# Optimization experiments

Measured on AMD Instinct MI355X. Metric: run time of the kernel, lower is better.

## Reference

```python
import jax, jax.numpy as jnp
import numpy as np

NUM_PER_SCALE = (64, 64, 64)   # static num_intervals_per_scale
DIST_BINS = 21
NUM_CLASSES = 5
D = 128   # node_embedding_dim
N = 512   # number of nodes (time frames)
KSIZE = 5


def _gru_last(x_seq, lens, Wih, Whh, bih, bhh):
    """Masked GRU over padded seqs; final hidden at each sequence's true length.
    x_seq: [I, T, F], lens: [I]. PyTorch GRU cell math."""
    I, T, _ = x_seq.shape
    H = Whh.shape[1]
    mask_t = (jnp.arange(T)[None, :] < lens[:, None]).T  # [T, I]

    def step(h, inp):
        x_t, m = inp
        gi = x_t @ Wih.T + bih            # [I, 3H]
        gh = h @ Whh.T + bhh
        ir, iz, in_ = jnp.split(gi, 3, axis=-1)
        hr, hz, hn = jnp.split(gh, 3, axis=-1)
        r = jax.nn.sigmoid(ir + hr)
        z = jax.nn.sigmoid(iz + hz)
        n = jnp.tanh(in_ + r * hn)
        h_new = (1.0 - z) * n + z * h
        return jnp.where(m[:, None], h_new, h), None

    h0 = jnp.zeros((I, H), x_seq.dtype)
    h_fin, _ = jax.lax.scan(step, h0, (jnp.swapaxes(x_seq, 0, 1), mask_t))
    return h_fin


def _bigru_last(x_pad, lens, Wih, Whh, bih, bhh):
    """Bidirectional GRU final hiddens, matching packed-sequence semantics."""
    hf = _gru_last(x_pad, lens, Wih[0], Whh[0], bih[0], bhh[0])
    T = x_pad.shape[1]
    t = jnp.arange(T)[None, :]
    rev = jnp.where(t < lens[:, None], lens[:, None] - 1 - t, t)  # reverse within valid length
    x_rev = jnp.take_along_axis(x_pad, rev[:, :, None], axis=1)
    hb = _gru_last(x_rev, lens, Wih[1], Whh[1], bih[1], bhh[1])
    return hf, hb


def reference(node_embeddings, time_positions, node_pred, audio_len,
              cur_anchor_intervals, smooth_kernel,
              feat_Wih, feat_Whh, feat_bih, feat_bhh,
              abn_Wih, abn_Whh, abn_bih, abn_bhh,
              start_w, end_w,
              uni_W1, uni_b1, uni_W2, uni_b2, uni_W3, uni_b3):
    n, d = node_embeddings.shape
    al = audio_len
    # temporal encoding
    freqs = jnp.linspace(0.0, 10.0, d)
    x = node_embeddings + 0.05 * jnp.sin(time_positions * freqs)  # [N, D]
    # grouped gaussian smoothing over time per class channel (symmetric kernel)
    pad = KSIZE // 2
    xp = jnp.pad(node_pred, ((pad, pad), (0, 0)))
    win = jnp.stack([xp[k:k + n] for k in range(KSIZE)])          # [K, N, C]
    smoothed = jax.nn.softmax(jnp.einsum('k,knc->nc', smooth_kernel, win), axis=-1)
    abnormal = smoothed[:, 0]                                     # normal_class_idx = 0
    tpos = time_positions[:, 0] * al                              # [N]

    bounds_list, conf_list, cls_list = [], [], []
    off = 0
    for s in range(3):
        ni = NUM_PER_SCALE[s]
        anc = cur_anchor_intervals[off:off + ni]
        off += ni
        starts, ends = anc[:, 0], anc[:, 1]
        mask = (tpos[None, :] >= starts[:, None]) & (tpos[None, :] <= ends[:, None])  # [ni, N]
        lens = mask.sum(axis=1)
        # stable gather: in-interval nodes first, original node order preserved
        key = jnp.where(mask, 0, n) + jnp.arange(n)[None, :]
        order = jnp.argsort(key, axis=1)
        x_pad = x[order]                       # [ni, N, D]
        abn_pad = abnormal[order][:, :, None]  # [ni, N, 1]
        hf, hb = _bigru_last(x_pad, lens, feat_Wih[s], feat_Whh[s], feat_bih[s], feat_bhh[s])
        af, ab = _bigru_last(abn_pad, lens, abn_Wih[s], abn_Whh[s], abn_bih[s], abn_bhh[s])
        local_feat = jnp.concatenate([hf, hb], axis=1)             # [ni, 2D]
        local_abn = (af[:, 0] + ab[:, 0]) * 0.5
        centers = (starts + ends) * 0.5
        widths = ends - starts
        sf = jnp.concatenate([local_feat, local_abn[:, None],
                              (centers / al)[:, None], (widths / al)[:, None]], axis=1)
        h = jax.nn.relu(sf @ uni_W1[s] + uni_b1[s])
        h = jax.nn.relu(h @ uni_W2[s] + uni_b2[s])   # dropout inactive (eval)
        out = h @ uni_W3[s] + uni_b3[s]
        sl = out[:, :DIST_BINS]
        el = out[:, DIST_BINS:2 * DIST_BINS]
        conf = out[:, 2 * DIST_BINS]
        cls = out[:, 2 * DIST_BINS + 1:]
        so = jax.nn.softmax(sl, axis=1) @ start_w[s]
        eo = jax.nn.softmax(el, axis=1) @ end_w[s]
        st = jnp.clip(starts + so, 0.0, al)
        en = jnp.clip(ends + eo, 0.0, al)
        bounds_list.append(jnp.stack([st, en], axis=1))
        conf_list.append(conf)
        cls_list.append(cls)
    return (jnp.concatenate(bounds_list, 0),
            jnp.concatenate(conf_list, 0),
            jnp.concatenate(cls_list, 0))


def setup_inputs():
    key = jax.random.key(0)
    ks = jax.random.split(key, 16)
    node_embeddings = jax.random.normal(ks[0], (N, D), dtype=jnp.float32)
    time_positions = jax.random.uniform(ks[1], (N, 1), dtype=jnp.float32)
    node_pred = jax.random.normal(ks[2], (N, NUM_CLASSES), dtype=jnp.float32)
    audio_len = jnp.ones((), jnp.float32)
    total = sum(NUM_PER_SCALE)
    st = jax.random.uniform(ks[3], (total,), minval=0.0, maxval=0.75)
    wd = jax.random.uniform(ks[4], (total,), minval=0.05, maxval=0.2)
    cur_anchor_intervals = jnp.stack([st, jnp.minimum(st + wd, 1.0)], axis=1)
    smooth_kernel = jnp.array([0.06136, 0.24477, 0.38774, 0.24477, 0.06136], jnp.float32)
    feat_Wih = 0.05 * jax.random.normal(ks[5], (3, 2, 3 * D, D))
    feat_Whh = 0.05 * jax.random.normal(ks[6], (3, 2, 3 * D, D))
    feat_bih = 0.05 * jax.random.normal(ks[7], (3, 2, 3 * D))
    feat_bhh = 0.05 * jax.random.normal(ks[8], (3, 2, 3 * D))
    abn_Wih = 0.5 * jax.random.normal(ks[9], (3, 2, 3, 1))
    abn_Whh = 0.5 * jax.random.normal(ks[10], (3, 2, 3, 1))
    abn_bih = 0.5 * jax.random.normal(ks[11], (3, 2, 3))
    abn_bhh = 0.5 * jax.random.normal(ks[12], (3, 2, 3))
    lin = jnp.linspace(-20.0, 20.0, DIST_BINS)
    start_w = jnp.tile(lin[None, :], (3, 1))
    end_w = jnp.tile(lin[None, :], (3, 1))
    fin = 2 * D + 3
    fout = 2 * DIST_BINS + 1 + (NUM_CLASSES - 1)
    uni_W1 = jax.random.normal(ks[13], (3, fin, 256)) / float(np.sqrt(fin))
    uni_b1 = jnp.zeros((3, 256), jnp.float32)
    uni_W2 = jax.random.normal(ks[14], (3, 256, 256)) / 16.0
    uni_b2 = jnp.zeros((3, 256), jnp.float32)
    uni_W3 = jax.random.normal(ks[15], (3, 256, fout)) / 16.0
    uni_b3 = jnp.zeros((3, fout), jnp.float32)
    return dict(node_embeddings=node_embeddings, time_positions=time_positions,
                node_pred=node_pred, audio_len=audio_len,
                cur_anchor_intervals=cur_anchor_intervals, smooth_kernel=smooth_kernel,
                feat_Wih=feat_Wih, feat_Whh=feat_Whh, feat_bih=feat_bih, feat_bhh=feat_bhh,
                abn_Wih=abn_Wih, abn_Whh=abn_Whh, abn_bih=abn_bih, abn_bhh=abn_bhh,
                start_w=start_w, end_w=end_w,
                uni_W1=uni_W1, uni_b1=uni_b1, uni_W2=uni_W2, uni_b2=uni_b2,
                uni_W3=uni_W3, uni_b3=uni_b3)
```

## Files before the change

### kernel.cpp

```cpp
#include <hip/hip_runtime.h>
#include <math.h>

#define N_NODES 512
#define DIM 128
#define NANCH 192
#define G3 384
#define FOUT 47
#define DBINS 21

__device__ __forceinline__ float fast_sigmoid(float x) {
    return __builtin_amdgcn_rcpf(1.f + __expf(-x));
}
__device__ __forceinline__ float fast_tanh(float x) {
    return 1.f - 2.f * __builtin_amdgcn_rcpf(1.f + __expf(2.f * x));
}

__global__ __launch_bounds__(384) void prep_kernel(
    const float* __restrict__ emb, const float* __restrict__ tpin,
    const float* __restrict__ Wih, const float* __restrict__ bih,
    const float* __restrict__ alp, const float* __restrict__ anchors,
    const float* __restrict__ npred, const float* __restrict__ skern,
    const float* __restrict__ aWih, const float* __restrict__ aWhh,
    const float* __restrict__ abih, const float* __restrict__ abhh,
    float* __restrict__ xW, int* __restrict__ members,
    int* __restrict__ lens, float* __restrict__ abn_res)
{
    int blk = blockIdx.x;
    int tid = threadIdx.x;
    if (blk < 192) {
        int sd = blk >> 5;
        int ng = blk & 31;
        __shared__ __align__(16) float xs[16][DIM];
        for (int idx = tid; idx < 16 * DIM; idx += 384) {
            int m = idx >> 7, k = idx & 127;
            int node = ng * 16 + m;
            float tv = tpin[node];
            float freq = 10.f * (float)k / 127.f;
            xs[m][k] = emb[node * DIM + k] + 0.05f * __sinf(tv * freq);
        }
        __syncthreads();
        float acc[16];
        float b = bih[sd * G3 + tid];
        #pragma unroll
        for (int m = 0; m < 16; ++m) acc[m] = b;
        const float* wrow = Wih + ((size_t)sd * G3 + tid) * DIM;
        for (int k = 0; k < DIM; k += 4) {
            float4 w4 = *(const float4*)(wrow + k);
            #pragma unroll
            for (int m = 0; m < 16; ++m) {
                float4 xv = *(const float4*)&xs[m][k];
                acc[m] = fmaf(w4.x, xv.x, acc[m]);
                acc[m] = fmaf(w4.y, xv.y, acc[m]);
                acc[m] = fmaf(w4.z, xv.z, acc[m]);
                acc[m] = fmaf(w4.w, xv.w, acc[m]);
            }
        }
        #pragma unroll
        for (int m = 0; m < 16; ++m)
            xW[((size_t)sd * N_NODES + ng * 16 + m) * G3 + tid] = acc[m];
    } else {
        int a = blk - 192;
        float al = alp[0];
        float s0 = anchors[a * 2 + 0];
        float e0 = anchors[a * 2 + 1];
        __shared__ int memloc[N_NODES];
        __shared__ float abn_lds[N_NODES];
        for (int node = tid; node < N_NODES; node += 384) {
            float sc[5];
            #pragma unroll
            for (int ch = 0; ch < 5; ++ch) {
                float acc = 0.f;
                #pragma unroll
                for (int k = 0; k < 5; ++k) {
                    int r = node + k - 2;
                    if (r >= 0 && r < N_NODES) acc += skern[k] * npred[r * 5 + ch];
                }
                sc[ch] = acc;
            }
            float m = sc[0];
            #pragma unroll
            for (int ch = 1; ch < 5; ++ch) m = fmaxf(m, sc[ch]);
            float sum = 0.f;
            #pragma unroll
            for (int ch = 0; ch < 5; ++ch) sum += __expf(sc[ch] - m);
            abn_lds[node] = __expf(sc[0] - m) / sum;
        }
        __syncthreads();
        if (tid < 64) {
            int lane = tid;
            int count = 0;
            for (int c = 0; c < N_NODES / 64; ++c) {
                int node = c * 64 + lane;
                float tp = tpin[node] * al;
                bool in = (tp >= s0) && (tp <= e0);
                unsigned long long m = __ballot(in);
                if (in) {
                    int pos = count + __popcll(m & ((1ull << lane) - 1ull));
                    members[a * N_NODES + pos] = node;
                    memloc[pos] = node;
                }
                count += __popcll(m);
            }
            if (lane == 0) lens[a] = count;
            int sc3 = a >> 6;
            float h = 0.f;
            if (lane < 2) {
                int sd = sc3 * 2 + lane;
                float wi0 = aWih[sd*3+0], wi1 = aWih[sd*3+1], wi2 = aWih[sd*3+2];
                float wh0 = aWhh[sd*3+0], wh1 = aWhh[sd*3+1], wh2 = aWhh[sd*3+2];
                float bi0 = abih[sd*3+0], bi1 = abih[sd*3+1], bi2 = abih[sd*3+2];
                float bh0 = abhh[sd*3+0], bh1 = abhh[sd*3+1], bh2 = abhh[sd*3+2];
                for (int t = 0; t < count; ++t) {
                    int idx = lane ? (count - 1 - t) : t;
                    float xv = abn_lds[memloc[idx]];
                    float r = fast_sigmoid(fmaf(wi0, xv, bi0) + fmaf(wh0, h, bh0));
                    float z = fast_sigmoid(fmaf(wi1, xv, bi1) + fmaf(wh1, h, bh1));
                    float nv = fast_tanh(fmaf(wi2, xv, bi2) + r * fmaf(wh2, h, bh2));
                    h = (1.f - z) * nv + z * h;
                }
            }
            float hb = __shfl(h, 1);
            if (lane == 0) abn_res[a] = 0.5f * (h + hb);
        }
    }
}

__global__ __launch_bounds__(512, 1) void gru_feat_kernel(
    const float* __restrict__ xW, const float* __restrict__ Whh,
    const float* __restrict__ bhh, const int* __restrict__ members,
    const int* __restrict__ lens, const float* __restrict__ anchors,
    float* __restrict__ feat_out)
{
    int b = blockIdx.x;
    int t0 = threadIdx.x;
    int j  = t0 >> 2;
    int s  = t0 & 3;

    __shared__ int perm_l[NANCH];
    if (t0 < NANCH) {
        float w = anchors[2 * t0 + 1] - anchors[2 * t0];
        int rank = 0;
        for (int q = 0; q < NANCH; ++q) {
            float wq = anchors[2 * q + 1] - anchors[2 * q];
            rank += (wq > w) || (wq == w && q < t0);
        }
        perm_l[rank] = t0;
    }
    __syncthreads();
    int a   = perm_l[b >> 1];
    int dir = b & 1;
    int sd  = (a >> 6) * 2 + dir;

    float wr[32], wz[32], wn[32];
    {
        const float* base = Whh + ((size_t)sd * G3) * DIM;
        const float* pr = base + (size_t)(j        ) * DIM + s * 32;
        const float* pz = base + (size_t)(j + DIM  ) * DIM + s * 32;
        const float* pn = base + (size_t)(j + 2*DIM) * DIM + s * 32;
        #pragma unroll
        for (int q = 0; q < 8; ++q) {
            float4 v = *(const float4*)(pr + 4 * q);
            wr[4*q+0]=v.x; wr[4*q+1]=v.y; wr[4*q+2]=v.z; wr[4*q+3]=v.w;
        }
        #pragma unroll
        for (int q = 0; q < 8; ++q) {
            float4 v = *(const float4*)(pz + 4 * q);
            wz[4*q+0]=v.x; wz[4*q+1]=v.y; wz[4*q+2]=v.z; wz[4*q+3]=v.w;
        }
        #pragma unroll
        for (int q = 0; q < 8; ++q) {
            float4 v = *(const float4*)(pn + 4 * q);
            wn[4*q+0]=v.x; wn[4*q+1]=v.y; wn[4*q+2]=v.z; wn[4*q+3]=v.w;
        }
    }
    #pragma unroll
    for (int q = 0; q < 32; ++q)
        asm volatile("" : "+v"(wr[q]), "+v"(wz[q]), "+v"(wn[q]));

    float bhr = bhh[sd * G3 + j];
    float bhz = bhh[sd * G3 + DIM + j];
    float bhn = bhh[sd * G3 + 2 * DIM + j];

    const float* xWp = xW + (size_t)sd * N_NODES * G3;
    const int* mem = members + a * N_NODES;
    int len = lens[a];

    __shared__ __align__(16) float hbuf[2][4][36];
    for (int i = t0; i < 2 * 4 * 36; i += 512) ((float*)hbuf)[i] = 0.f;
    __syncthreads();

    int node0 = (len > 0) ? mem[dir ? (len - 1) : 0] : 0;
    float gr = xWp[(size_t)node0 * G3 + j];
    float gz = xWp[(size_t)node0 * G3 + DIM + j];
    float gn = xWp[(size_t)node0 * G3 + 2 * DIM + j];

    int cur = 0;
    for (int t = 0; t < len; ++t) {
        float gr_n = 0.f, gz_n = 0.f, gn_n = 0.f;
        if (t + 1 < len) {
            int nn = mem[dir ? (len - 2 - t) : (t + 1)];
            gr_n = xWp[(size_t)nn * G3 + j];
            gz_n = xWp[(size_t)nn * G3 + DIM + j];
            gn_n = xWp[(size_t)nn * G3 + 2 * DIM + j];
        }
        float ar = 0.f, az = 0.f, an_ = 0.f;
        const float4* hp = (const float4*)(&hbuf[cur][s][0]);
        #pragma unroll
        for (int q = 0; q < 8; ++q) {
            float4 hv = hp[q];
            ar = fmaf(wr[4*q+0], hv.x, ar); ar = fmaf(wr[4*q+1], hv.y, ar);
            ar = fmaf(wr[4*q+2], hv.z, ar); ar = fmaf(wr[4*q+3], hv.w, ar);
            az = fmaf(wz[4*q+0], hv.x, az); az = fmaf(wz[4*q+1], hv.y, az);
            az = fmaf(wz[4*q+2], hv.z, az); az = fmaf(wz[4*q+3], hv.w, az);
            an_ = fmaf(wn[4*q+0], hv.x, an_); an_ = fmaf(wn[4*q+1], hv.y, an_);
            an_ = fmaf(wn[4*q+2], hv.z, an_); an_ = fmaf(wn[4*q+3], hv.w, an_);
        }
        ar  += __shfl_xor(ar, 1);  ar  += __shfl_xor(ar, 2);
        az  += __shfl_xor(az, 1);  az  += __shfl_xor(az, 2);
        an_ += __shfl_xor(an_, 1); an_ += __shfl_xor(an_, 2);

        float r  = fast_sigmoid(gr + ar + bhr);
        float z  = fast_sigmoid(gz + az + bhz);
        float nv = fast_tanh(gn + r * (an_ + bhn));
        float hj = hbuf[cur][j >> 5][j & 31];
        float hnew = (1.f - z) * nv + z * hj;
        if (s == 0) hbuf[cur ^ 1][j >> 5][j & 31] = hnew;
        __syncthreads();
        cur ^= 1;
        gr = gr_n; gz = gz_n; gn = gn_n;
    }
    if (s == 0) feat_out[a * 256 + dir * DIM + j] = hbuf[cur][j >> 5][j & 31];
}

__global__ __launch_bounds__(256) void head_kernel(
    const float* __restrict__ feat, const float* __restrict__ abn_res,
    const float* __restrict__ anchors, const float* __restrict__ alp,
    const float* __restrict__ W1, const float* __restrict__ b1,
    const float* __restrict__ W2, const float* __restrict__ b2,
    const float* __restrict__ W3, const float* __restrict__ b3,
    const float* __restrict__ sw, const float* __restrict__ ew,
    float* __restrict__ out)
{
    int a = blockIdx.x;
    int tid = threadIdx.x;
    int s = a >> 6;
    __shared__ float sf[260];
    __shared__ float h1[256];
    __shared__ float h2[256];
    __shared__ float o[FOUT];
    float al = alp[0];
    float st = anchors[a * 2 + 0];
    float en = anchors[a * 2 + 1];
    sf[tid] = feat[a * 256 + tid];
    if (tid == 0) {
        sf[256] = abn_res[a];
        sf[257] = (st + en) * 0.5f / al;
        sf[258] = (en - st) / al;
    }
    __syncthreads();

    const float* w1 = W1 + (size_t)s * 259 * 256;
    float acc = b1[s * 256 + tid];
    for (int jj = 0; jj < 259; ++jj) acc = fmaf(sf[jj], w1[jj * 256 + tid], acc);
    h1[tid] = fmaxf(acc, 0.f);
    __syncthreads();

    const float* w2 = W2 + (size_t)s * 256 * 256;
    acc = b2[s * 256 + tid];
    for (int jj = 0; jj < 256; ++jj) acc = fmaf(h1[jj], w2[jj * 256 + tid], acc);
    h2[tid] = fmaxf(acc, 0.f);
    __syncthreads();

    if (tid < FOUT) {
        const float* w3 = W3 + (size_t)s * 256 * FOUT;
        acc = b3[s * FOUT + tid];
        for (int jj = 0; jj < 256; ++jj) acc = fmaf(h2[jj], w3[jj * FOUT + tid], acc);
        o[tid] = acc;
    }
    __syncthreads();

    if (tid < 2) {
        const float* lw = (tid == 0) ? (sw + s * DBINS) : (ew + s * DBINS);
        const float* sl = o + tid * DBINS;
        float m = sl[0];
        for (int jj = 1; jj < DBINS; ++jj) m = fmaxf(m, sl[jj]);
        float sum = 0.f, dot = 0.f;
        for (int jj = 0; jj < DBINS; ++jj) {
            float e = __expf(sl[jj] - m);
            sum += e;
            dot = fmaf(e, lw[jj], dot);
        }
        float off = dot / sum;
        float base = (tid == 0) ? st : en;
        out[a * 2 + tid] = fminf(fmaxf(base + off, 0.f), al);
    }
    if (tid == 42) out[2 * NANCH + a] = o[42];
    if (tid >= 43 && tid < FOUT) out[3 * NANCH + a * 4 + (tid - 43)] = o[tid];
}

extern "C" void kernel_launch(void* const* d_in, const int* in_sizes, int n_in,
                              void* d_out, int out_size, void* d_ws, size_t ws_size,
                              hipStream_t stream) {
    const float* emb   = (const float*)d_in[0];
    const float* tpin  = (const float*)d_in[1];
    const float* npred = (const float*)d_in[2];
    const float* alp   = (const float*)d_in[3];
    const float* anch  = (const float*)d_in[4];
    const float* skern = (const float*)d_in[5];
    const float* fWih  = (const float*)d_in[6];
    const float* fWhh  = (const float*)d_in[7];
    const float* fbih  = (const float*)d_in[8];
    const float* fbhh  = (const float*)d_in[9];
    const float* aWih  = (const float*)d_in[10];
    const float* aWhh  = (const float*)d_in[11];
    const float* abih  = (const float*)d_in[12];
    const float* abhh  = (const float*)d_in[13];
    const float* sw    = (const float*)d_in[14];
    const float* ew    = (const float*)d_in[15];
    const float* W1    = (const float*)d_in[16];
    const float* b1    = (const float*)d_in[17];
    const float* W2    = (const float*)d_in[18];
    const float* b2    = (const float*)d_in[19];
    const float* W3    = (const float*)d_in[20];
    const float* b3    = (const float*)d_in[21];

    float* ws = (float*)d_ws;
    float* xW       = ws;
    float* abn_res  = ws + 1179648;
    float* feat     = ws + 1179904;
    int*   members  = (int*)(ws + 1229056);
    int*   lens     = (int*)(ws + 1327360);
    float* outp     = (float*)d_out;

    prep_kernel<<<384, 384, 0, stream>>>(emb, tpin, fWih, fbih, alp, anch, npred, skern,
                                         aWih, aWhh, abih, abhh,
                                         xW, members, lens, abn_res);
    gru_feat_kernel<<<2 * NANCH, 512, 0, stream>>>(xW, fWhh, fbhh, members, lens, anch, feat);
    head_kernel<<<NANCH, 256, 0, stream>>>(feat, abn_res, anch, alp,
                                           W1, b1, W2, b2, W3, b3, sw, ew, outp);
}
```

Before: 243.2 us.

## Batch two anchors per GRU block, staging recurrent weights in LDS

Each GRU block now processes two anchors of the same scale and direction, paired by width rank within their scale, so the per-step weight reads are shared across two hidden states. The r and z recurrent weights move from registers into padded LDS, and the n weights are re-read from global memory every step. The grid is halved to 192 blocks, and per-sequence length masking is added so paired sequences of different lengths run in lockstep. The aim is to halve the number of serial blocks and reuse weights, at the cost of more LDS and global traffic per step and wasted steps when the paired lengths differ.

```diff
diff --git a/kernel.cpp b/kernel.cpp
--- a/kernel.cpp
+++ b/kernel.cpp
@@ -7,6 +7,7 @@
 #define G3 384
 #define FOUT 47
 #define DBINS 21
+#define WPAD 132
 
 __device__ __forceinline__ float fast_sigmoid(float x) {
     return __builtin_amdgcn_rcpf(1.f + __expf(-x));
@@ -125,111 +126,141 @@
     }
 }
 
-__global__ __launch_bounds__(512, 1) void gru_feat_kernel(
+__global__ __launch_bounds__(512) void gru_feat_kernel(
     const float* __restrict__ xW, const float* __restrict__ Whh,
     const float* __restrict__ bhh, const int* __restrict__ members,
     const int* __restrict__ lens, const float* __restrict__ anchors,
     float* __restrict__ feat_out)
 {
-    int b = blockIdx.x;
+    int bb = blockIdx.x;
     int t0 = threadIdx.x;
     int j  = t0 >> 2;
     int s  = t0 & 3;
-
-    __shared__ int perm_l[NANCH];
-    if (t0 < NANCH) {
-        float w = anchors[2 * t0 + 1] - anchors[2 * t0];
+    int sc  = bb >> 6;
+    int idx = bb & 63;
+    int dir = idx & 1;
+    int pr  = idx >> 1;
+    int sd  = sc * 2 + dir;
+
+    __shared__ __align__(16) float ldsW[2 * DIM * WPAD];
+    __shared__ __align__(16) float hbA[2][4][36];
+    __shared__ __align__(16) float hbB[2][4][36];
+    __shared__ int perm_l[64];
+
+    if (t0 < 64) {
+        int aa = sc * 64 + t0;
+        float w = anchors[2 * aa + 1] - anchors[2 * aa];
         int rank = 0;
-        for (int q = 0; q < NANCH; ++q) {
-            float wq = anchors[2 * q + 1] - anchors[2 * q];
+        for (int q = 0; q < 64; ++q) {
+            int aq = sc * 64 + q;
+            float wq = anchors[2 * aq + 1] - anchors[2 * aq];
             rank += (wq > w) || (wq == w && q < t0);
         }
-        perm_l[rank] = t0;
-    }
-    __syncthreads();
-    int a   = perm_l[b >> 1];
-    int dir = b & 1;
-    int sd  = (a >> 6) * 2 + dir;
-
-    float wr[32], wz[32], wn[32];
-    {
-        const float* base = Whh + ((size_t)sd * G3) * DIM;
-        const float* pr = base + (size_t)(j        ) * DIM + s * 32;
-        const float* pz = base + (size_t)(j + DIM  ) * DIM + s * 32;
-        const float* pn = base + (size_t)(j + 2*DIM) * DIM + s * 32;
-        #pragma unroll
-        for (int q = 0; q < 8; ++q) {
-            float4 v = *(const float4*)(pr + 4 * q);
-            wr[4*q+0]=v.x; wr[4*q+1]=v.y; wr[4*q+2]=v.z; wr[4*q+3]=v.w;
-        }
-        #pragma unroll
-        for (int q = 0; q < 8; ++q) {
-            float4 v = *(const float4*)(pz + 4 * q);
-            wz[4*q+0]=v.x; wz[4*q+1]=v.y; wz[4*q+2]=v.z; wz[4*q+3]=v.w;
-        }
-        #pragma unroll
-        for (int q = 0; q < 8; ++q) {
-            float4 v = *(const float4*)(pn + 4 * q);
-            wn[4*q+0]=v.x; wn[4*q+1]=v.y; wn[4*q+2]=v.z; wn[4*q+3]=v.w;
-        }
-    }
-    #pragma unroll
-    for (int q = 0; q < 32; ++q)
-        asm volatile("" : "+v"(wr[q]), "+v"(wz[q]), "+v"(wn[q]));
+        perm_l[rank] = aa;
+    }
+    const float* wbase = Whh + (size_t)sd * G3 * DIM;
+    for (int i = t0; i < 2 * DIM * 32; i += 512) {
+        int row = i >> 5, c = (i & 31) << 2;
+        *(float4*)&ldsW[row * WPAD + c] = *(const float4*)(wbase + row * DIM + c);
+    }
+    for (int i = t0; i < 2 * 4 * 36; i += 512) { ((float*)hbA)[i] = 0.f; ((float*)hbB)[i] = 0.f; }
+    __syncthreads();
+
+    int a0 = perm_l[2 * pr], a1 = perm_l[2 * pr + 1];
 
     float bhr = bhh[sd * G3 + j];
     float bhz = bhh[sd * G3 + DIM + j];
     float bhn = bhh[sd * G3 + 2 * DIM + j];
 
     const float* xWp = xW + (size_t)sd * N_NODES * G3;
-    const int* mem = members + a * N_NODES;
-    int len = lens[a];
-
-    __shared__ __align__(16) float hbuf[2][4][36];
-    for (int i = t0; i < 2 * 4 * 36; i += 512) ((float*)hbuf)[i] = 0.f;
-    __syncthreads();
-
-    int node0 = (len > 0) ? mem[dir ? (len - 1) : 0] : 0;
-    float gr = xWp[(size_t)node0 * G3 + j];
-    float gz = xWp[(size_t)node0 * G3 + DIM + j];
-    float gn = xWp[(size_t)node0 * G3 + 2 * DIM + j];
+    const int* memA = members + a0 * N_NODES;  int lenA = lens[a0];
+    const int* memB = members + a1 * N_NODES;  int lenB = lens[a1];
+    int T = lenA > lenB ? lenA : lenB;
+
+    int n0A = (lenA > 0) ? memA[dir ? (lenA - 1) : 0] : 0;
+    float grA = xWp[(size_t)n0A * G3 + j];
+    float gzA = xWp[(size_t)n0A * G3 + DIM + j];
+    float gnA = xWp[(size_t)n0A * G3 + 2 * DIM + j];
+    int n0B = (lenB > 0) ? memB[dir ? (lenB - 1) : 0] : 0;
+    float grB = xWp[(size_t)n0B * G3 + j];
+    float gzB = xWp[(size_t)n0B * G3 + DIM + j];
+    float gnB = xWp[(size_t)n0B * G3 + 2 * DIM + j];
+
+    const float4* wr4 = (const float4*)&ldsW[(size_t)j * WPAD + s * 32];
+    const float4* wz4 = (const float4*)&ldsW[(size_t)(DIM + j) * WPAD + s * 32];
+    const float4* wnp = (const float4*)(wbase + (size_t)(2 * DIM + j) * DIM + s * 32);
 
     int cur = 0;
-    for (int t = 0; t < len; ++t) {
-        float gr_n = 0.f, gz_n = 0.f, gn_n = 0.f;
-        if (t + 1 < len) {
-            int nn = mem[dir ? (len - 2 - t) : (t + 1)];
-            gr_n = xWp[(size_t)nn * G3 + j];
-            gz_n = xWp[(size_t)nn * G3 + DIM + j];
-            gn_n = xWp[(size_t)nn * G3 + 2 * DIM + j];
-        }
-        float ar = 0.f, az = 0.f, an_ = 0.f;
-        const float4* hp = (const float4*)(&hbuf[cur][s][0]);
+    for (int t = 0; t < T; ++t) {
+        float4 wnv[8];
+        #pragma unroll
+        for (int q = 0; q < 8; ++q) wnv[q] = wnp[q];
+        float grA_n = 0.f, gzA_n = 0.f, gnA_n = 0.f;
+        float grB_n = 0.f, gzB_n = 0.f, gnB_n = 0.f;
+        if (t + 1 < lenA) {
+            int nn = memA[dir ? (lenA - 2 - t) : (t + 1)];
+            grA_n = xWp[(size_t)nn * G3 + j];
+            gzA_n = xWp[(size_t)nn * G3 + DIM + j];
+            gnA_n = xWp[(size_t)nn * G3 + 2 * DIM + j];
+        }
+        if (t + 1 < lenB) {
+            int nn = memB[dir ? (lenB - 2 - t) : (t + 1)];
+            grB_n = xWp[(size_t)nn * G3 + j];
+            gzB_n = xWp[(size_t)nn * G3 + DIM + j];
+            gnB_n = xWp[(size_t)nn * G3 + 2 * DIM + j];
+        }
+        float arA = 0.f, azA = 0.f, anA = 0.f, arB = 0.f, azB = 0.f, anB = 0.f;
+        const float4* hA4 = (const float4*)&hbA[cur][s][0];
+        const float4* hB4 = (const float4*)&hbB[cur][s][0];
         #pragma unroll
         for (int q = 0; q < 8; ++q) {
-            float4 hv = hp[q];
-            ar = fmaf(wr[4*q+0], hv.x, ar); ar = fmaf(wr[4*q+1], hv.y, ar);
-            ar = fmaf(wr[4*q+2], hv.z, ar); ar = fmaf(wr[4*q+3], hv.w, ar);
-            az = fmaf(wz[4*q+0], hv.x, az); az = fmaf(wz[4*q+1], hv.y, az);
-            az = fmaf(wz[4*q+2], hv.z, az); az = fmaf(wz[4*q+3], hv.w, az);
-            an_ = fmaf(wn[4*q+0], hv.x, an_); an_ = fmaf(wn[4*q+1], hv.y, an_);
-            an_ = fmaf(wn[4*q+2], hv.z, an_); an_ = fmaf(wn[4*q+3], hv.w, an_);
-        }
-        ar  += __shfl_xor(ar, 1);  ar  += __shfl_xor(ar, 2);
-        az  += __shfl_xor(az, 1);  az  += __shfl_xor(az, 2);
-        an_ += __shfl_xor(an_, 1); an_ += __shfl_xor(an_, 2);
-
-        float r  = fast_sigmoid(gr + ar + bhr);
-        float z  = fast_sigmoid(gz + az + bhz);
-        float nv = fast_tanh(gn + r * (an_ + bhn));
-        float hj = hbuf[cur][j >> 5][j & 31];
-        float hnew = (1.f - z) * nv + z * hj;
-        if (s == 0) hbuf[cur ^ 1][j >> 5][j & 31] = hnew;
+            float4 wv = wr4[q], zv = wz4[q], nv = wnv[q];
+            float4 ha = hA4[q], hb = hB4[q];
+            arA = fmaf(wv.x, ha.x, arA); arA = fmaf(wv.y, ha.y, arA);
+            arA = fmaf(wv.z, ha.z, arA); arA = fmaf(wv.w, ha.w, arA);
+            azA = fmaf(zv.x, ha.x, azA); azA = fmaf(zv.y, ha.y, azA);
+            azA = fmaf(zv.z, ha.z, azA); azA = fmaf(zv.w, ha.w, azA);
+            anA = fmaf(nv.x, ha.x, anA); anA = fmaf(nv.y, ha.y, anA);
+            anA = fmaf(nv.z, ha.z, anA); anA = fmaf(nv.w, ha.w, anA);
+            arB = fmaf(wv.x, hb.x, arB); arB = fmaf(wv.y, hb.y, arB);
+            arB = fmaf(wv.z, hb.z, arB); arB = fmaf(wv.w, hb.w, arB);
+            azB = fmaf(zv.x, hb.x, azB); azB = fmaf(zv.y, hb.y, azB);
+            azB = fmaf(zv.z, hb.z, azB); azB = fmaf(zv.w, hb.w, azB);
+            anB = fmaf(nv.x, hb.x, anB); anB = fmaf(nv.y, hb.y, anB);
+            anB = fmaf(nv.z, hb.z, anB); anB = fmaf(nv.w, hb.w, anB);
+        }
+        arA += __shfl_xor(arA, 1); arA += __shfl_xor(arA, 2);
+        azA += __shfl_xor(azA, 1); azA += __shfl_xor(azA, 2);
+        anA += __shfl_xor(anA, 1); anA += __shfl_xor(anA, 2);
+        arB += __shfl_xor(arB, 1); arB += __shfl_xor(arB, 2);
+        azB += __shfl_xor(azB, 1); azB += __shfl_xor(azB, 2);
+        anB += __shfl_xor(anB, 1); anB += __shfl_xor(anB, 2);
+
+        float rA = fast_sigmoid(grA + arA + bhr);
+        float zA = fast_sigmoid(gzA + azA + bhz);
+        float nA = fast_tanh(gnA + rA * (anA + bhn));
+        float hjA = hbA[cur][j >> 5][j & 31];
+        float hnA = (t < lenA) ? ((1.f - zA) * nA + zA * hjA) : hjA;
+
+        float rB = fast_sigmoid(grB + arB + bhr);
+        float zB = fast_sigmoid(gzB + azB + bhz);
+        float nB = fast_tanh(gnB + rB * (anB + bhn));
+        float hjB = hbB[cur][j >> 5][j & 31];
+        float hnB = (t < lenB) ? ((1.f - zB) * nB + zB * hjB) : hjB;
+
+        if (s == 0) {
+            hbA[cur ^ 1][j >> 5][j & 31] = hnA;
+            hbB[cur ^ 1][j >> 5][j & 31] = hnB;
+        }
         __syncthreads();
         cur ^= 1;
-        gr = gr_n; gz = gz_n; gn = gn_n;
-    }
-    if (s == 0) feat_out[a * 256 + dir * DIM + j] = hbuf[cur][j >> 5][j & 31];
+        grA = grA_n; gzA = gzA_n; gnA = gnA_n;
+        grB = grB_n; gzB = gzB_n; gnB = gnB_n;
+    }
+    if (s == 0) {
+        feat_out[a0 * 256 + dir * DIM + j] = hbA[cur][j >> 5][j & 31];
+        feat_out[a1 * 256 + dir * DIM + j] = hbB[cur][j >> 5][j & 31];
+    }
 }
 
 __global__ __launch_bounds__(256) void head_kernel(
@@ -335,7 +366,7 @@
     prep_kernel<<<384, 384, 0, stream>>>(emb, tpin, fWih, fbih, alp, anch, npred, skern,
                                          aWih, aWhh, abih, abhh,
                                          xW, members, lens, abn_res);
-    gru_feat_kernel<<<2 * NANCH, 512, 0, stream>>>(xW, fWhh, fbhh, members, lens, anch, feat);
+    gru_feat_kernel<<<NANCH, 512, 0, stream>>>(xW, fWhh, fbhh, members, lens, anch, feat);
     head_kernel<<<NANCH, 256, 0, stream>>>(feat, abn_res, anch, alp,
                                            W1, b1, W2, b2, W3, b3, sw, ew, outp);
 }
```

Result: slower. 320.7 us (+31.9%).
